# Performance work log

Measured on AMD Instinct MI355X. Metric: run time of the kernel, lower is better.

The kernel has to match this reference:

```python
import jax, jax.numpy as jnp
import numpy as np

EMBED_DIM = 768
NUM_HEADS = 12
HEAD_DIM = EMBED_DIM // NUM_HEADS
MLP_HIDDEN = int(EMBED_DIM * 4.0)
LN_EPS = 1e-5


def setup_inputs() -> dict:
    key = jax.random.key(0)
    ks = jax.random.split(key, 8)
    C, H = EMBED_DIM, MLP_HIDDEN
    s = 0.02
    return {
        "x": jax.random.normal(ks[0], (2, 2048, C), dtype=jnp.float32),
        "ln1_g": jnp.ones((C,), jnp.float32),
        "ln1_b": jnp.zeros((C,), jnp.float32),
        "qkv_w": jax.random.normal(ks[1], (3 * C, C), jnp.float32) * s,
        "proj_w": jax.random.normal(ks[2], (C, C), jnp.float32) * s,
        "proj_b": jnp.zeros((C,), jnp.float32),
        "ln2_g": jnp.ones((C,), jnp.float32),
        "ln2_b": jnp.zeros((C,), jnp.float32),
        "fc1_w": jax.random.normal(ks[3], (H, C), jnp.float32) * s,
        "fc1_b": jnp.zeros((H,), jnp.float32),
        "fc2_w": jax.random.normal(ks[4], (C, H), jnp.float32) * s,
        "fc2_b": jnp.zeros((C,), jnp.float32),
    }


def _layernorm(x, g, b):
    mu = jnp.mean(x, axis=-1, keepdims=True)
    var = jnp.mean(jnp.square(x - mu), axis=-1, keepdims=True)
    return (x - mu) * jax.lax.rsqrt(var + LN_EPS) * g + b


def reference(x, ln1_g, ln1_b, qkv_w, proj_w, proj_b, ln2_g, ln2_b,
              fc1_w, fc1_b, fc2_w, fc2_b):
    B, N, C = x.shape
    Hh, Dh = NUM_HEADS, HEAD_DIM
    scale = Dh ** -0.5

    # --- attention branch (pre-norm) ---
    h = _layernorm(x, ln1_g, ln1_b)
    qkv = h @ qkv_w.T                                   # [B,N,3C]
    qkv = qkv.reshape(B, N, 3, Hh, Dh)
    q = qkv[:, :, 0].transpose(0, 2, 1, 3)              # [B,H,N,D]
    k = qkv[:, :, 1].transpose(0, 2, 1, 3)
    v = qkv[:, :, 2].transpose(0, 2, 1, 3)
    attn = jnp.einsum('bhnd,bhmd->bhnm', q, k) * scale  # [B,H,N,N]
    attn = jax.nn.softmax(attn, axis=-1)
    o = jnp.einsum('bhnm,bhmd->bhnd', attn, v)          # [B,H,N,D]
    o = o.transpose(0, 2, 1, 3).reshape(B, N, C)
    x = x + o @ proj_w.T + proj_b

    # --- MLP branch (pre-norm), exact GELU like nn.GELU ---
    h = _layernorm(x, ln2_g, ln2_b)
    h = jax.nn.gelu(h @ fc1_w.T + fc1_b, approximate=False)
    x = x + h @ fc2_w.T + fc2_b
    return x
```

## Files before the change

kernel.cpp:

```cpp
#include <hip/hip_runtime.h>
#include <hip/hip_bf16.h>
#include <cstdint>
#include <math.h>


typedef __bf16 bf16_t;
typedef bf16_t bf16x4 __attribute__((ext_vector_type(4)));
typedef bf16_t bf16x8 __attribute__((ext_vector_type(8)));
typedef float floatx4 __attribute__((ext_vector_type(4)));

#define AS1 __attribute__((address_space(1)))
#define AS3 __attribute__((address_space(3)))

__device__ __forceinline__ void async_load16(const void* g, void* l) {
  const AS1 unsigned int* gp =
      reinterpret_cast<const AS1 unsigned int*>(reinterpret_cast<uintptr_t>(g));
  AS3 unsigned int* lp = reinterpret_cast<AS3 unsigned int*>(
      static_cast<unsigned int>(reinterpret_cast<uintptr_t>(l)));
  __builtin_amdgcn_global_load_lds(gp, lp, 16, 0, 0);
}

__device__ __forceinline__ bf16x8 lds_read8(const bf16_t* p) {
  return *reinterpret_cast<const bf16x8*>(p);
}

__global__ __launch_bounds__(256) void cvt_k(const float* __restrict__ in,
                                             bf16_t* __restrict__ out, int n4) {
  const int i = blockIdx.x * 256 + threadIdx.x;
  if (i < n4) {
    const float4 v = reinterpret_cast<const float4*>(in)[i];
    bf16x4 o;
    o[0] = (bf16_t)v.x; o[1] = (bf16_t)v.y; o[2] = (bf16_t)v.z; o[3] = (bf16_t)v.w;
    reinterpret_cast<bf16x4*>(out)[i] = o;
  }
}

__global__ __launch_bounds__(256) void cvt_all_k(
    const float* __restrict__ s0, const float* __restrict__ s1,
    const float* __restrict__ s2, const float* __restrict__ s3,
    bf16_t* __restrict__ d0, bf16_t* __restrict__ d1, bf16_t* __restrict__ d2,
    bf16_t* __restrict__ d3) {
  int i = blockIdx.x * 256 + threadIdx.x;
  const float* src;
  bf16_t* dst;
  if (i < 442368) { src = s0; dst = d0; }
  else if (i < 589824) { src = s1; dst = d1; i -= 442368; }
  else if (i < 1179648) { src = s2; dst = d2; i -= 589824; }
  else if (i < 1769472) { src = s3; dst = d3; i -= 1179648; }
  else return;
  const float4 v = reinterpret_cast<const float4*>(src)[i];
  bf16x4 o;
  o[0] = (bf16_t)v.x; o[1] = (bf16_t)v.y; o[2] = (bf16_t)v.z; o[3] = (bf16_t)v.w;
  reinterpret_cast<bf16x4*>(dst)[i] = o;
}

template <int INIT>
__global__ __launch_bounds__(256) void ln_k(const float* __restrict__ x,
                                            const float* __restrict__ g,
                                            const float* __restrict__ b,
                                            bf16_t* __restrict__ out,
                                            const float* __restrict__ b2,
                                            float* __restrict__ oinit) {
  const int row = blockIdx.x;
  const int tid = threadIdx.x;
  const float* xr = x + (long)row * 768;
  float v[3];
#pragma unroll
  for (int e = 0; e < 3; e++) v[e] = xr[tid + e * 256];
  float s = v[0] + v[1] + v[2];
  float ss = v[0] * v[0] + v[1] * v[1] + v[2] * v[2];
#pragma unroll
  for (int off = 32; off >= 1; off >>= 1) {
    s += __shfl_down(s, off, 64);
    ss += __shfl_down(ss, off, 64);
  }
  __shared__ float red[8];
  __shared__ float stat[2];
  const int wv = tid >> 6;
  if ((tid & 63) == 0) { red[wv] = s; red[4 + wv] = ss; }
  __syncthreads();
  if (tid == 0) {
    float S = red[0] + red[1] + red[2] + red[3];
    float SS = red[4] + red[5] + red[6] + red[7];
    float mu = S * (1.0f / 768.0f);
    float var = SS * (1.0f / 768.0f) - mu * mu;
    stat[0] = mu;
    stat[1] = rsqrtf(var + 1e-5f);
  }
  __syncthreads();
  const float mu = stat[0], rs = stat[1];
#pragma unroll
  for (int e = 0; e < 3; e++) {
    int c = tid + e * 256;
    out[(long)row * 768 + c] = (bf16_t)((v[e] - mu) * rs * g[c] + b[c]);
    if constexpr (INIT == 1) oinit[(long)row * 768 + c] = v[e] + b2[c];
  }
}

template <int MODE>
__global__ __launch_bounds__(256, 2) void gemm_k(
    const bf16_t* __restrict__ A, const bf16_t* __restrict__ Bt, int lda,
    int ldb, int keff, int Nld, const float* __restrict__ bias,
    bf16_t* __restrict__ out_bf, bf16_t* __restrict__ q_out,
    bf16_t* __restrict__ k_out, bf16_t* __restrict__ vt_out) {
  constexpr int BK = 32;
  __shared__ __align__(16) bf16_t As[2][128 * BK];
  __shared__ __align__(16) bf16_t Bs[2][128 * BK];

  const int tid = threadIdx.x;
  const int w = tid >> 6;
  const int lane = tid & 63;
  const int quad = lane >> 4;
  const int lid = lane & 15;
  const int wr = (w >> 1) * 64;
  const int wc = (w & 1) * 64;
  const int mBase = blockIdx.y * 128;
  const int nBase = blockIdx.x * 128;

  const int ldsRowSub = lane >> 2;
  const int kblk = (lane & 3) ^ (ldsRowSub & 3);
  const int rq0 = (quad ^ (lid & 3)) * 8;
  const int c0 = w * 2, c1 = w * 2 + 1;
  const int rowA0 = c0 * 16 + ldsRowSub, rowA1 = c1 * 16 + ldsRowSub;

  const bf16_t* Ag = A + (long)mBase * lda;
  const bf16_t* Bg = Bt + (long)nBase * ldb;

  floatx4 acc[4][4];
#pragma unroll
  for (int i = 0; i < 4; i++)
#pragma unroll
    for (int j = 0; j < 4; j++) acc[i][j] = (floatx4){0.f, 0.f, 0.f, 0.f};

  async_load16(Ag + (long)rowA0 * lda + kblk * 8, &As[0][c0 * 512]);
  async_load16(Ag + (long)rowA1 * lda + kblk * 8, &As[0][c1 * 512]);
  async_load16(Bg + (long)rowA0 * ldb + kblk * 8, &Bs[0][c0 * 512]);
  async_load16(Bg + (long)rowA1 * ldb + kblk * 8, &Bs[0][c1 * 512]);

  const int iters = keff / BK;
  int cur = 0;
  for (int it = 0; it < iters; it++) {
    __syncthreads();
    if (it + 1 < iters) {
      const int k0 = (it + 1) * BK;
      const int nb = cur ^ 1;
      async_load16(Ag + (long)rowA0 * lda + k0 + kblk * 8, &As[nb][c0 * 512]);
      async_load16(Ag + (long)rowA1 * lda + k0 + kblk * 8, &As[nb][c1 * 512]);
      async_load16(Bg + (long)rowA0 * ldb + k0 + kblk * 8, &Bs[nb][c0 * 512]);
      async_load16(Bg + (long)rowA1 * ldb + k0 + kblk * 8, &Bs[nb][c1 * 512]);
    }

    bf16x8 af[4], bfv[4];
#pragma unroll
    for (int i = 0; i < 4; i++)
      af[i] = lds_read8(&As[cur][(wr + i * 16 + lid) * BK + rq0]);
#pragma unroll
    for (int j = 0; j < 4; j++)
      bfv[j] = lds_read8(&Bs[cur][(wc + j * 16 + lid) * BK + rq0]);
#pragma unroll
    for (int i = 0; i < 4; i++)
#pragma unroll
      for (int j = 0; j < 4; j++)
        acc[i][j] = __builtin_amdgcn_mfma_f32_16x16x32_bf16(af[i], bfv[j],
                                                            acc[i][j], 0, 0, 0);
    cur ^= 1;
  }

#pragma unroll
  for (int i = 0; i < 4; i++) {
    const int mRow = mBase + wr + i * 16 + quad * 4;
#pragma unroll
    for (int j = 0; j < 4; j++) {
      const int n = nBase + wc + j * 16 + lid;
      if constexpr (MODE == 0) {
        const int which = n / 768;
        const int rem = n - which * 768;
        const int head = rem >> 6;
        const int d = rem & 63;
        const int b = mRow >> 11;
        const int t = mRow & 2047;
        const int bh = b * 12 + head;
        if (which == 2) {
          bf16x4 pk;
#pragma unroll
          for (int r = 0; r < 4; r++) pk[r] = (bf16_t)acc[i][j][r];
          const long off = ((long)bh * 64 + d) * 2048 + t;
          *reinterpret_cast<bf16x4*>(&vt_out[off]) = pk;
        } else if (which == 0) {
#pragma unroll
          for (int r = 0; r < 4; r++)
            q_out[((long)bh * 2048 + t + r) * 64 + d] =
                (bf16_t)(acc[i][j][r] * 0.125f);
        } else {
#pragma unroll
          for (int r = 0; r < 4; r++)
            k_out[((long)bh * 2048 + t + r) * 64 + d] = (bf16_t)acc[i][j][r];
        }
      } else {
        const float bv = bias[n];
#pragma unroll
        for (int r = 0; r < 4; r++) {
          float v = acc[i][j][r] + bv;
          float ge = 0.5f * v * (1.0f + erff(v * 0.70710678118654752f));
          out_bf[(long)(mRow + r) * Nld + n] = (bf16_t)ge;
        }
      }
    }
  }
}

template <int MODE>
__global__ __launch_bounds__(256, 4) void gemm64_k(
    const bf16_t* __restrict__ A, const bf16_t* __restrict__ Bt, int lda,
    int ldb, int keff, int Nld, const float* __restrict__ bias,
    const float* __restrict__ resid_f, float* __restrict__ out_f) {
  constexpr int BK = 32;
  __shared__ __align__(16) bf16_t As[2][128 * BK];
  __shared__ __align__(16) bf16_t Bs[2][64 * BK];

  const int tid = threadIdx.x;
  const int w = tid >> 6;
  const int lane = tid & 63;
  const int quad = lane >> 4;
  const int lid = lane & 15;
  const int mBase = blockIdx.y * 128;
  const int nBase = blockIdx.x * 64;
  const int kOff = blockIdx.z * keff;

  const int ldsRowSub = lane >> 2;
  const int kblk = (lane & 3) ^ (ldsRowSub & 3);
  const int rq0 = (quad ^ (lid & 3)) * 8;
  const int rowA0 = w * 16 + ldsRowSub;
  const int rowA1 = (w + 4) * 16 + ldsRowSub;

  const bf16_t* Ag = A + (long)mBase * lda + kOff;
  const bf16_t* Bg = Bt + (long)nBase * ldb + kOff;

  floatx4 acc[2][4];
#pragma unroll
  for (int i = 0; i < 2; i++)
#pragma unroll
    for (int j = 0; j < 4; j++) acc[i][j] = (floatx4){0.f, 0.f, 0.f, 0.f};

  async_load16(Ag + (long)rowA0 * lda + kblk * 8, &As[0][w * 512]);
  async_load16(Ag + (long)rowA1 * lda + kblk * 8, &As[0][(w + 4) * 512]);
  async_load16(Bg + (long)rowA0 * ldb + kblk * 8, &Bs[0][w * 512]);

  const int iters = keff / BK;
  int cur = 0;
  for (int it = 0; it < iters; it++) {
    __syncthreads();
    if (it + 1 < iters) {
      const int k0 = (it + 1) * BK;
      const int nb = cur ^ 1;
      async_load16(Ag + (long)rowA0 * lda + k0 + kblk * 8, &As[nb][w * 512]);
      async_load16(Ag + (long)rowA1 * lda + k0 + kblk * 8, &As[nb][(w + 4) * 512]);
      async_load16(Bg + (long)rowA0 * ldb + k0 + kblk * 8, &Bs[nb][w * 512]);
    }

    bf16x8 af[2], bfv[4];
#pragma unroll
    for (int i = 0; i < 2; i++)
      af[i] = lds_read8(&As[cur][(w * 32 + i * 16 + lid) * BK + rq0]);
#pragma unroll
    for (int j = 0; j < 4; j++)
      bfv[j] = lds_read8(&Bs[cur][(j * 16 + lid) * BK + rq0]);
#pragma unroll
    for (int i = 0; i < 2; i++)
#pragma unroll
      for (int j = 0; j < 4; j++)
        acc[i][j] = __builtin_amdgcn_mfma_f32_16x16x32_bf16(af[i], bfv[j],
                                                            acc[i][j], 0, 0, 0);
    cur ^= 1;
  }

#pragma unroll
  for (int i = 0; i < 2; i++) {
    const int mRow = mBase + w * 32 + i * 16 + quad * 4;
#pragma unroll
    for (int j = 0; j < 4; j++) {
      const int n = nBase + j * 16 + lid;
      if constexpr (MODE == 1) {
        const float bv = bias[n];
#pragma unroll
        for (int r = 0; r < 4; r++) {
          const long off = (long)(mRow + r) * Nld + n;
          out_f[off] = resid_f[off] + acc[i][j][r] + bv;
        }
      } else {
#pragma unroll
        for (int r = 0; r < 4; r++) {
          const long off = (long)(mRow + r) * Nld + n;
          unsafeAtomicAdd(&out_f[off], acc[i][j][r]);
        }
      }
    }
  }
}

__global__ __launch_bounds__(512, 1) void flash_k(const bf16_t* __restrict__ q,
                                                  const bf16_t* __restrict__ kk,
                                                  const bf16_t* __restrict__ vt,
                                                  bf16_t* __restrict__ U,
                                                  float* __restrict__ lbuf) {
  constexpr int SK = 64, D = 64;
  __shared__ __align__(16) bf16_t Ks[2][SK * D];
  __shared__ __align__(16) bf16_t Vs[2][D * SK];

  const int tid = threadIdx.x;
  const int w = tid >> 6;
  const int lane = tid & 63;
  const int quad = lane >> 4;
  const int lid = lane & 15;
  const int bh = blockIdx.y;
  const int half = blockIdx.z;
  const int qBase = blockIdx.x * 128;

  const bf16_t* qg = q + ((long)bh * 2048 + qBase) * D;
  const bf16_t* kg = kk + ((long)bh * 2048 + half * 1024) * D;
  const bf16_t* vg = vt + (long)bh * D * 2048 + half * 1024;

  bf16x8 aq[2];
#pragma unroll
  for (int k2 = 0; k2 < 2; k2++)
    aq[k2] = *reinterpret_cast<const bf16x8*>(qg + (w * 16 + lid) * D +
                                              k2 * 32 + quad * 8);

  const int srow = lane >> 3;
  const int sdb = (lane & 7) ^ srow;
  const int rsw = lid & 7;

  async_load16(kg + (long)(w * 8 + srow) * D + sdb * 8, &Ks[0][w * 512]);
  async_load16(vg + (long)(w * 8 + srow) * 2048 + sdb * 8, &Vs[0][w * 512]);

  float lsum = 0.f;
  floatx4 oacc[4];
#pragma unroll
  for (int jo = 0; jo < 4; jo++) oacc[jo] = (floatx4){0.f, 0.f, 0.f, 0.f};

  int cur = 0;
  for (int kci = 0; kci < 16; kci++) {
    __syncthreads();
    if (kci + 1 < 16) {
      const int kc = (kci + 1) * 64;
      const int nb = cur ^ 1;
      async_load16(kg + (long)(kc + w * 8 + srow) * D + sdb * 8, &Ks[nb][w * 512]);
      async_load16(vg + (long)(w * 8 + srow) * 2048 + kc + sdb * 8, &Vs[nb][w * 512]);
    }

    floatx4 sacc[4];
#pragma unroll
    for (int jm = 0; jm < 4; jm++) sacc[jm] = (floatx4){0.f, 0.f, 0.f, 0.f};
#pragma unroll
    for (int k2 = 0; k2 < 2; k2++) {
#pragma unroll
      for (int jm = 0; jm < 4; jm++) {
        const bf16x8 ak = lds_read8(
            &Ks[cur][(jm * 16 + lid) * D + (((k2 * 4 + quad) ^ rsw) * 8)]);
        sacc[jm] =
            __builtin_amdgcn_mfma_f32_16x16x32_bf16(ak, aq[k2], sacc[jm], 0, 0, 0);
      }
    }

    bf16x8 ap[2];
#pragma unroll
    for (int k2 = 0; k2 < 2; k2++) {
      uint32_t pk[2][2];
#pragma unroll
      for (int j = 0; j < 2; j++) {
        const int jm = k2 * 2 + j;
        const float p0 = exp2f(fmaf(sacc[jm][0], 1.44269504f, -11.5415603f));
        const float p1 = exp2f(fmaf(sacc[jm][1], 1.44269504f, -11.5415603f));
        const float p2 = exp2f(fmaf(sacc[jm][2], 1.44269504f, -11.5415603f));
        const float p3 = exp2f(fmaf(sacc[jm][3], 1.44269504f, -11.5415603f));
        lsum += ((p0 + p1) + p2) + p3;
        asm("v_cvt_pk_bf16_f32 %0, %1, %2" : "=v"(pk[j][0]) : "v"(p0), "v"(p1));
        asm("v_cvt_pk_bf16_f32 %0, %1, %2" : "=v"(pk[j][1]) : "v"(p2), "v"(p3));
      }
      asm("v_permlane32_swap_b32 %0, %1" : "+v"(pk[0][0]), "+v"(pk[1][0]));
      asm("v_permlane16_swap_b32 %0, %1" : "+v"(pk[0][0]), "+v"(pk[1][0]));
      asm("v_permlane32_swap_b32 %0, %1" : "+v"(pk[0][1]), "+v"(pk[1][1]));
      asm("v_permlane16_swap_b32 %0, %1" : "+v"(pk[0][1]), "+v"(pk[1][1]));
      union { uint32_t u[4]; bf16x8 v; } au;
      au.u[0] = pk[0][0];
      au.u[1] = pk[0][1];
      au.u[2] = pk[1][0];
      au.u[3] = pk[1][1];
      ap[k2] = au.v;
    }

#pragma unroll
    for (int k2 = 0; k2 < 2; k2++) {
#pragma unroll
      for (int jo = 0; jo < 4; jo++) {
        const bf16x8 bv = lds_read8(
            &Vs[cur][(jo * 16 + lid) * SK + (((k2 * 4 + quad) ^ rsw) * 8)]);
        oacc[jo] =
            __builtin_amdgcn_mfma_f32_16x16x32_bf16(ap[k2], bv, oacc[jo], 0, 0, 0);
      }
    }
    cur ^= 1;
  }

  lsum += __shfl_xor(lsum, 16, 64);
  lsum += __shfl_xor(lsum, 32, 64);

  const long lrow = ((long)half * 24 + bh) * 2048 + qBase + w * 16;
  if (quad == 0) lbuf[lrow + lid] = lsum;

  bf16_t* Ub = U + (((long)half * 24 + bh) * 2048 + qBase) * D;
#pragma unroll
  for (int jo = 0; jo < 4; jo++) {
#pragma unroll
    for (int r = 0; r < 4; r++) {
      const int t = w * 16 + quad * 4 + r;
      Ub[(long)t * D + jo * 16 + lid] = (bf16_t)oacc[jo][r];
    }
  }
}

__global__ __launch_bounds__(256) void combine_k(const bf16_t* __restrict__ U,
                                                 const float* __restrict__ lbuf,
                                                 bf16_t* __restrict__ o) {
  const int idx = blockIdx.x * 256 + threadIdx.x;
  const int bh = idx >> 17;
  const int rem = idx & 131071;
  const int t = rem >> 6;
  const int d = rem & 63;
  const float l0 = lbuf[bh * 2048 + t];
  const float l1 = lbuf[(24 + bh) * 2048 + t];
  const float u = (float)U[idx] + (float)U[3145728 + idx];
  const int b = bh / 12;
  const int head = bh - b * 12;
  o[((long)b * 2048 + t) * 768 + head * 64 + d] = (bf16_t)(u / (l0 + l1));
}

extern "C" void kernel_launch(void* const* d_in, const int* in_sizes, int n_in,
                              void* d_out, int out_size, void* d_ws,
                              size_t ws_size, hipStream_t stream) {
  (void)in_sizes; (void)n_in; (void)out_size;
  const float* x = (const float*)d_in[0];
  const float* ln1_g = (const float*)d_in[1];
  const float* ln1_b = (const float*)d_in[2];
  const float* qkv_w = (const float*)d_in[3];
  const float* proj_w = (const float*)d_in[4];
  const float* proj_b = (const float*)d_in[5];
  const float* ln2_g = (const float*)d_in[6];
  const float* ln2_b = (const float*)d_in[7];
  const float* fc1_w = (const float*)d_in[8];
  const float* fc1_b = (const float*)d_in[9];
  const float* fc2_w = (const float*)d_in[10];
  const float* fc2_b = (const float*)d_in[11];
  float* out = (float*)d_out;
  char* ws = (char*)d_ws;

  const bool big = ws_size >= (size_t)64487424;

  if (big) {
    bf16_t* wqkv = (bf16_t*)(ws + 0);
    bf16_t* wproj = (bf16_t*)(ws + 3538944);
    bf16_t* wfc1 = (bf16_t*)(ws + 4718592);
    bf16_t* wfc2 = (bf16_t*)(ws + 9437184);
    bf16_t* h1 = (bf16_t*)(ws + 14155776);
    bf16_t* ob = h1;
    bf16_t* qb = (bf16_t*)(ws + 20447232);
    bf16_t* kb = (bf16_t*)(ws + 26738688);
    bf16_t* vtb = (bf16_t*)(ws + 33030144);
    bf16_t* Ubuf = (bf16_t*)(ws + 39321600);
    float* lbuf = (float*)(ws + 51904512);
    float* x1 = (float*)(ws + 20447232);
    bf16_t* h2 = (bf16_t*)(ws + 33030144);
    bf16_t* hg = (bf16_t*)(ws + 39321600);

    cvt_all_k<<<6912, 256, 0, stream>>>(qkv_w, proj_w, fc1_w, fc2_w, wqkv,
                                        wproj, wfc1, wfc2);
    ln_k<0><<<4096, 256, 0, stream>>>(x, ln1_g, ln1_b, h1, nullptr, nullptr);
    gemm_k<0><<<dim3(18, 32), 256, 0, stream>>>(h1, wqkv, 768, 768, 768, 2304,
                                                nullptr, nullptr, qb, kb, vtb);
    flash_k<<<dim3(16, 24, 2), 512, 0, stream>>>(qb, kb, vtb, Ubuf, lbuf);
    combine_k<<<12288, 256, 0, stream>>>(Ubuf, lbuf, ob);
    gemm64_k<1><<<dim3(12, 32), 256, 0, stream>>>(ob, wproj, 768, 768, 768, 768,
                                                  proj_b, x, x1);
    ln_k<1><<<4096, 256, 0, stream>>>(x1, ln2_g, ln2_b, h2, fc2_b, out);
    gemm_k<2><<<dim3(24, 32), 256, 0, stream>>>(h2, wfc1, 768, 768, 768, 3072,
                                                fc1_b, hg, nullptr, nullptr,
                                                nullptr);
    gemm64_k<6><<<dim3(12, 32, 2), 256, 0, stream>>>(hg, wfc2, 3072, 3072, 1536,
                                                     768, nullptr, nullptr, out);
  } else {
    bf16_t* wqkv = (bf16_t*)(ws + 0);
    bf16_t* wproj = (bf16_t*)(ws + 3538944);
    bf16_t* h1 = (bf16_t*)(ws + 4718592);
    bf16_t* ob = h1;
    bf16_t* qb = (bf16_t*)(ws + 11010048);
    bf16_t* kb = (bf16_t*)(ws + 17301504);
    bf16_t* vtb = (bf16_t*)(ws + 23592960);
    float* x1 = (float*)(ws + 11010048);
    bf16_t* h2 = (bf16_t*)(ws + 23592960);
    bf16_t* wfc1 = (bf16_t*)(ws + 0);
    bf16_t* wfc2 = (bf16_t*)(ws + 4718592);
    bf16_t* hg = (bf16_t*)(ws + 29884416);
    bf16_t* Ubuf = (bf16_t*)(ws + 29884416);
    float* lbuf = (float*)(ws + 42467328);

    cvt_k<<<1728, 256, 0, stream>>>(qkv_w, wqkv, 442368);
    cvt_k<<<576, 256, 0, stream>>>(proj_w, wproj, 147456);
    ln_k<0><<<4096, 256, 0, stream>>>(x, ln1_g, ln1_b, h1, nullptr, nullptr);
    gemm_k<0><<<dim3(18, 32), 256, 0, stream>>>(h1, wqkv, 768, 768, 768, 2304,
                                                nullptr, nullptr, qb, kb, vtb);
    flash_k<<<dim3(16, 24, 2), 512, 0, stream>>>(qb, kb, vtb, Ubuf, lbuf);
    combine_k<<<12288, 256, 0, stream>>>(Ubuf, lbuf, ob);
    gemm64_k<1><<<dim3(12, 32), 256, 0, stream>>>(ob, wproj, 768, 768, 768, 768,
                                                  proj_b, x, x1);
    cvt_k<<<2304, 256, 0, stream>>>(fc1_w, wfc1, 589824);
    cvt_k<<<2304, 256, 0, stream>>>(fc2_w, wfc2, 589824);
    ln_k<1><<<4096, 256, 0, stream>>>(x1, ln2_g, ln2_b, h2, fc2_b, out);
    for (int h = 0; h < 2; h++) {
      gemm_k<2><<<dim3(12, 32), 256, 0, stream>>>(
          h2, wfc1 + (long)h * 1536 * 768, 768, 768, 768, 1536,
          fc1_b + h * 1536, hg, nullptr, nullptr, nullptr);
      gemm64_k<6><<<dim3(12, 32), 256, 0, stream>>>(hg, wfc2 + h * 1536, 1536,
                                                    3072, 1536, 768, nullptr,
                                                    nullptr, out);
    }
  }
}
```

Before: 295.2 us.

## Triple-buffer GEMM LDS tiles with partial vmcnt waits

After: 288.3 us. -2.3%, faster.

```diff
diff --git a/kernel.cpp b/kernel.cpp
--- a/kernel.cpp
+++ b/kernel.cpp
@@ -104,8 +104,8 @@
     bf16_t* __restrict__ out_bf, bf16_t* __restrict__ q_out,
     bf16_t* __restrict__ k_out, bf16_t* __restrict__ vt_out) {
   constexpr int BK = 32;
-  __shared__ __align__(16) bf16_t As[2][128 * BK];
-  __shared__ __align__(16) bf16_t Bs[2][128 * BK];
+  __shared__ __align__(16) bf16_t As[3][128 * BK];
+  __shared__ __align__(16) bf16_t Bs[3][128 * BK];
 
   const int tid = threadIdx.x;
   const int w = tid >> 6;
@@ -132,22 +132,27 @@
 #pragma unroll
     for (int j = 0; j < 4; j++) acc[i][j] = (floatx4){0.f, 0.f, 0.f, 0.f};
 
-  async_load16(Ag + (long)rowA0 * lda + kblk * 8, &As[0][c0 * 512]);
-  async_load16(Ag + (long)rowA1 * lda + kblk * 8, &As[0][c1 * 512]);
-  async_load16(Bg + (long)rowA0 * ldb + kblk * 8, &Bs[0][c0 * 512]);
-  async_load16(Bg + (long)rowA1 * ldb + kblk * 8, &Bs[0][c1 * 512]);
+  auto stage = [&](int b, int k0) {
+    async_load16(Ag + (long)rowA0 * lda + k0 + kblk * 8, &As[b][c0 * 512]);
+    async_load16(Ag + (long)rowA1 * lda + k0 + kblk * 8, &As[b][c1 * 512]);
+    async_load16(Bg + (long)rowA0 * ldb + k0 + kblk * 8, &Bs[b][c0 * 512]);
+    async_load16(Bg + (long)rowA1 * ldb + k0 + kblk * 8, &Bs[b][c1 * 512]);
+  };
 
   const int iters = keff / BK;
+  stage(0, 0);
+  stage(1, BK);
+
   int cur = 0;
   for (int it = 0; it < iters; it++) {
-    __syncthreads();
-    if (it + 1 < iters) {
-      const int k0 = (it + 1) * BK;
-      const int nb = cur ^ 1;
-      async_load16(Ag + (long)rowA0 * lda + k0 + kblk * 8, &As[nb][c0 * 512]);
-      async_load16(Ag + (long)rowA1 * lda + k0 + kblk * 8, &As[nb][c1 * 512]);
-      async_load16(Bg + (long)rowA0 * ldb + k0 + kblk * 8, &Bs[nb][c0 * 512]);
-      async_load16(Bg + (long)rowA1 * ldb + k0 + kblk * 8, &Bs[nb][c1 * 512]);
+    if (it + 1 < iters)
+      asm volatile("s_waitcnt vmcnt(4) lgkmcnt(0)" ::: "memory");
+    else
+      asm volatile("s_waitcnt vmcnt(0) lgkmcnt(0)" ::: "memory");
+    __builtin_amdgcn_s_barrier();
+    if (it + 2 < iters) {
+      int nb = cur + 2; if (nb >= 3) nb -= 3;
+      stage(nb, (it + 2) * BK);
     }
 
     bf16x8 af[4], bfv[4];
@@ -163,7 +168,7 @@
       for (int j = 0; j < 4; j++)
         acc[i][j] = __builtin_amdgcn_mfma_f32_16x16x32_bf16(af[i], bfv[j],
                                                             acc[i][j], 0, 0, 0);
-    cur ^= 1;
+    cur = (cur == 2) ? 0 : cur + 1;
   }
 
 #pragma unroll
@@ -215,8 +220,8 @@
     int ldb, int keff, int Nld, const float* __restrict__ bias,
     const float* __restrict__ resid_f, float* __restrict__ out_f) {
   constexpr int BK = 32;
-  __shared__ __align__(16) bf16_t As[2][128 * BK];
-  __shared__ __align__(16) bf16_t Bs[2][64 * BK];
+  __shared__ __align__(16) bf16_t As[3][128 * BK];
+  __shared__ __align__(16) bf16_t Bs[3][64 * BK];
 
   const int tid = threadIdx.x;
   const int w = tid >> 6;
@@ -242,20 +247,26 @@
 #pragma unroll
     for (int j = 0; j < 4; j++) acc[i][j] = (floatx4){0.f, 0.f, 0.f, 0.f};
 
-  async_load16(Ag + (long)rowA0 * lda + kblk * 8, &As[0][w * 512]);
-  async_load16(Ag + (long)rowA1 * lda + kblk * 8, &As[0][(w + 4) * 512]);
-  async_load16(Bg + (long)rowA0 * ldb + kblk * 8, &Bs[0][w * 512]);
+  auto stage = [&](int b, int k0) {
+    async_load16(Ag + (long)rowA0 * lda + k0 + kblk * 8, &As[b][w * 512]);
+    async_load16(Ag + (long)rowA1 * lda + k0 + kblk * 8, &As[b][(w + 4) * 512]);
+    async_load16(Bg + (long)rowA0 * ldb + k0 + kblk * 8, &Bs[b][w * 512]);
+  };
 
   const int iters = keff / BK;
+  stage(0, 0);
+  stage(1, BK);
+
   int cur = 0;
   for (int it = 0; it < iters; it++) {
-    __syncthreads();
-    if (it + 1 < iters) {
-      const int k0 = (it + 1) * BK;
-      const int nb = cur ^ 1;
-      async_load16(Ag + (long)rowA0 * lda + k0 + kblk * 8, &As[nb][w * 512]);
-      async_load16(Ag + (long)rowA1 * lda + k0 + kblk * 8, &As[nb][(w + 4) * 512]);
-      async_load16(Bg + (long)rowA0 * ldb + k0 + kblk * 8, &Bs[nb][w * 512]);
+    if (it + 1 < iters)
+      asm volatile("s_waitcnt vmcnt(3) lgkmcnt(0)" ::: "memory");
+    else
+      asm volatile("s_waitcnt vmcnt(0) lgkmcnt(0)" ::: "memory");
+    __builtin_amdgcn_s_barrier();
+    if (it + 2 < iters) {
+      int nb = cur + 2; if (nb >= 3) nb -= 3;
+      stage(nb, (it + 2) * BK);
     }
 
     bf16x8 af[2], bfv[4];
@@ -271,7 +282,7 @@
       for (int j = 0; j < 4; j++)
         acc[i][j] = __builtin_amdgcn_mfma_f32_16x16x32_bf16(af[i], bfv[j],
                                                             acc[i][j], 0, 0, 0);
-    cur ^= 1;
+    cur = (cur == 2) ? 0 : cur + 1;
   }
 
 #pragma unroll
```
